# Kernel tuning notes

Measured on AMD Instinct MI355X. Metric: run time of the kernel, lower is better.

Reference implementation:

```python
import jax, jax.numpy as jnp
import numpy as np


def setup_inputs() -> dict:
    key = jax.random.key(0)
    B, C, H, W = 32, 256, 64, 64
    x = jax.random.normal(key, (B, C, H, W), dtype=jnp.float32)
    adj = jnp.ones((C, C), dtype=jnp.float32)
    para = jnp.ones((1, C, H, W), dtype=jnp.float32)
    return {"x": x, "adj": adj, "para": para}


def reference(x, adj, para):
    B, C, H, W = x.shape
    fea = x.reshape(B, C, H * W)                     # [B, C, HW]
    c_adj = jnp.mean(x, axis=(2, 3))                 # global avg pool -> [B, C]
    # pairwise sigmoid-difference similarity, batched over B
    d = c_adj[:, None, :] - c_adj[:, :, None]        # t1 - t2: [B, C(i=row from t2), C(j=col from t1)]
    s = jnp.abs(jnp.abs(jax.nn.sigmoid(d) - 0.5) - 0.5) * 2.0
    s = (s + jnp.swapaxes(s, 1, 2)) * 0.5            # symmetrize
    w = adj[None, :, :] * s                          # [B, C, C]
    out = jnp.einsum('bij,bjk->bik', w, fea)         # small GEMM per sample
    out = out.reshape(B, C, H, W) * para             # elementwise scale
    return jax.nn.relu(out)
```

## Files before the change

### kernel.cpp

```cpp
#include <hip/hip_runtime.h>
#include <math.h>

#define BB 32
#define CC 256
#define HWW 4096

typedef unsigned short u16;
typedef unsigned int u32;

typedef __attribute__((ext_vector_type(8))) short bf16x8;
typedef __attribute__((ext_vector_type(4))) float f32x4;

__device__ inline u16 f2bf(float f) {
    u32 u = __float_as_uint(f);
    u32 r = (u + 0x7fff + ((u >> 16) & 1)) >> 16;
    return (u16)r;
}


__global__ __launch_bounds__(256) void pool_transpose_kernel(const float* __restrict__ x,
                                                             u16* __restrict__ xT,
                                                             float* __restrict__ partial) {
    int b  = blockIdx.z;
    int c0 = blockIdx.y * 64;
    int h0 = blockIdx.x * 64;
    const float* xB = x + (size_t)b * CC * HWW;

    __shared__ float tile[64][65];
    __shared__ float psum[64];
    int t  = threadIdx.x;
    int cl = t >> 4;
    int h4 = (t & 15) * 4;

#pragma unroll
    for (int m = 0; m < 4; ++m) {
        int c = cl + 16 * m;
        float4 v = *(const float4*)&xB[(size_t)(c0 + c) * HWW + h0 + h4];
        tile[c][h4 + 0] = v.x;
        tile[c][h4 + 1] = v.y;
        tile[c][h4 + 2] = v.z;
        tile[c][h4 + 3] = v.w;
        float s = v.x + v.y + v.z + v.w;
#pragma unroll
        for (int off = 8; off > 0; off >>= 1)
            s += __shfl_down(s, off, 16);
        if ((t & 15) == 0) psum[c] = s;
    }
    __syncthreads();

    if (t < 64)
        partial[((size_t)b * 64 + blockIdx.x) * CC + c0 + t] = psum[t];

    int hl = t >> 2;
    int cq = (t & 3) * 16;
    u32 p0 = (u32)f2bf(tile[cq + 0][hl]) | ((u32)f2bf(tile[cq + 1][hl]) << 16);
    u32 p1 = (u32)f2bf(tile[cq + 2][hl]) | ((u32)f2bf(tile[cq + 3][hl]) << 16);
    u32 p2 = (u32)f2bf(tile[cq + 4][hl]) | ((u32)f2bf(tile[cq + 5][hl]) << 16);
    u32 p3 = (u32)f2bf(tile[cq + 6][hl]) | ((u32)f2bf(tile[cq + 7][hl]) << 16);
    u32 p4 = (u32)f2bf(tile[cq + 8][hl]) | ((u32)f2bf(tile[cq + 9][hl]) << 16);
    u32 p5 = (u32)f2bf(tile[cq +10][hl]) | ((u32)f2bf(tile[cq +11][hl]) << 16);
    u32 p6 = (u32)f2bf(tile[cq +12][hl]) | ((u32)f2bf(tile[cq +13][hl]) << 16);
    u32 p7 = (u32)f2bf(tile[cq +14][hl]) | ((u32)f2bf(tile[cq +15][hl]) << 16);
    u16* dst = xT + ((size_t)b * HWW + h0 + hl) * CC + c0 + cq;
    *(uint4*)(dst)     = make_uint4(p0, p1, p2, p3);
    *(uint4*)(dst + 8) = make_uint4(p4, p5, p6, p7);
}


__global__ __launch_bounds__(256) void reduce_kernel(const float* __restrict__ partial,
                                                     float* __restrict__ c_adj) {
    int b = blockIdx.x;
    int c = threadIdx.x;
    float s = 0.f;
#pragma unroll 8
    for (int hx = 0; hx < 64; ++hx)
        s += partial[((size_t)b * 64 + hx) * CC + c];
    c_adj[b * CC + c] = s * (1.0f / HWW);
}


__global__ __launch_bounds__(256) void weight_bf16_kernel(const float* __restrict__ c_adj,
                                                          const float* __restrict__ adj,
                                                          u16* __restrict__ wb) {
    int idx = blockIdx.x * 256 + threadIdx.x;
    int b = idx >> 16;
    int rem = idx & 65535;
    int i = rem >> 8;
    int j = rem & 255;
    float d = c_adj[b * CC + j] - c_adj[b * CC + i];
    float tt = expf(-fabsf(d));
    float s = 2.f * tt / (1.f + tt);
    wb[idx] = f2bf(adj[i * CC + j] * s);
}

#define GBM 128
#define GBN 128
#define GBK 32

__global__ __launch_bounds__(256) void mfma_gemm_kernel(const u16* __restrict__ wb,
                                                        const u16* __restrict__ xT,
                                                        const float* __restrict__ para,
                                                        float* __restrict__ out) {
    int b  = blockIdx.z;
    int i0 = blockIdx.y * GBM;
    int n0 = blockIdx.x * GBN;
    const u16* wB = wb + (size_t)b * CC * CC;
    const u16* xB = xT + (size_t)b * HWW * CC;

    __shared__ u16 lds[2][2][4096];

    int t    = threadIdx.x;
    int lane = t & 63;
    int wid  = t >> 6;
    int wr   = wid >> 1;
    int wc   = wid & 1;

    f32x4 acc[4][4] = {};

    int r0  = t >> 2;
    int c0q = t & 3;
    int cs  = c0q ^ ((r0 >> 1) & 3);
    int e0 = r0 * 32 + 8 * cs;
    int e1 = (r0 + 64) * 32 + 8 * cs;

    const u16* gA0 = wB + (size_t)(i0 + r0) * CC + 8 * c0q;
    const u16* gA1 = wB + (size_t)(i0 + r0 + 64) * CC + 8 * c0q;
    const u16* gB0 = xB + (size_t)(n0 + r0) * CC + 8 * c0q;
    const u16* gB1 = xB + (size_t)(n0 + r0 + 64) * CC + 8 * c0q;

    uint4 ra0, ra1, rb0, rb1;

#define LOADT(kk) { ra0 = *(const uint4*)(gA0 + (kk)); ra1 = *(const uint4*)(gA1 + (kk)); \
                    rb0 = *(const uint4*)(gB0 + (kk)); rb1 = *(const uint4*)(gB1 + (kk)); }
#define STORET(bf) { *(uint4*)&lds[bf][0][e0] = ra0; *(uint4*)&lds[bf][0][e1] = ra1; \
                     *(uint4*)&lds[bf][1][e0] = rb0; *(uint4*)&lds[bf][1][e1] = rb1; }

    LOADT(0);
    STORET(0);
    __syncthreads();

    int lrow = lane & 15;
    int kc   = lane >> 4;
    int swz  = (lrow >> 1) & 3;

#pragma unroll 1
    for (int kt = 0; kt < 8; ++kt) {
        int cur = kt & 1;
        if (kt < 7) LOADT((kt + 1) * GBK);

        bf16x8 af[4], bfr[4];
#pragma unroll
        for (int m = 0; m < 4; ++m) {
            int row = wr * 64 + m * 16 + lrow;
            af[m] = *(bf16x8*)&lds[cur][0][row * 32 + 8 * (kc ^ swz)];
        }
#pragma unroll
        for (int q = 0; q < 4; ++q) {
            int row = wc * 64 + q * 16 + lrow;
            bfr[q] = *(bf16x8*)&lds[cur][1][row * 32 + 8 * (kc ^ swz)];
        }
#pragma unroll
        for (int m = 0; m < 4; ++m)
#pragma unroll
            for (int q = 0; q < 4; ++q)
                acc[m][q] = __builtin_amdgcn_mfma_f32_16x16x32_bf16(af[m], bfr[q], acc[m][q], 0, 0, 0);

        if (kt < 7) STORET(cur ^ 1);
        __syncthreads();
    }
#undef LOADT
#undef STORET

    int dcol = lane & 15;
    int drow = 4 * (lane >> 4);
#pragma unroll
    for (int m = 0; m < 4; ++m) {
#pragma unroll
        for (int q = 0; q < 4; ++q) {
            int i = i0 + wr * 64 + m * 16 + drow;
            int n = n0 + wc * 64 + q * 16 + dcol;
#pragma unroll
            for (int r = 0; r < 4; ++r) {
                float pv = para[(size_t)(i + r) * HWW + n];
                float o = fmaxf(acc[m][q][r] * pv, 0.f);
                __builtin_nontemporal_store(o, &out[((size_t)b * CC + i + r) * HWW + n]);
            }
        }
    }
}


__global__ __launch_bounds__(256) void avgpool_kernel(const float* __restrict__ x,
                                                      float* __restrict__ c_adj) {
    int bc = blockIdx.x;
    const float4* p4 = (const float4*)(x + (size_t)bc * HWW);
    int t = threadIdx.x;
    float sum = 0.f;
#pragma unroll
    for (int m = 0; m < 4; ++m) {
        float4 v = p4[t + 256 * m];
        sum += v.x + v.y + v.z + v.w;
    }
#pragma unroll
    for (int off = 32; off > 0; off >>= 1)
        sum += __shfl_down(sum, off, 64);
    __shared__ float partial[4];
    int wid = t >> 6, lane = t & 63;
    if (lane == 0) partial[wid] = sum;
    __syncthreads();
    if (t == 0)
        c_adj[bc] = (partial[0] + partial[1] + partial[2] + partial[3]) * (1.0f / HWW);
}

__global__ __launch_bounds__(256) void weight_kernel(const float* __restrict__ c_adj,
                                                     const float* __restrict__ adj,
                                                     float* __restrict__ w) {
    int idx = blockIdx.x * 256 + threadIdx.x;
    int b = idx >> 16, rem = idx & 65535, i = rem >> 8, j = rem & 255;
    float d = c_adj[b * CC + j] - c_adj[b * CC + i];
    float tt = expf(-fabsf(d));
    w[idx] = adj[i * CC + j] * 2.f * tt / (1.f + tt);
}

#define BM 64
#define BN 64
#define BK 16
__global__ __launch_bounds__(256) void gemm_kernel(const float* __restrict__ w,
                                                   const float* __restrict__ x,
                                                   const float* __restrict__ para,
                                                   float* __restrict__ out) {
    int b = blockIdx.z, i0 = blockIdx.y * BM, n0 = blockIdx.x * BN;
    const float* wB = w + (size_t)b * CC * CC;
    const float* xB = x + (size_t)b * CC * HWW;
    float* outB = out + (size_t)b * CC * HWW;
    __shared__ float wT[BK][68];
    __shared__ float xS[BK][BN];
    int t = threadIdx.x, tr = t >> 4, tc = t & 15;
    float acc[4][4] = {};
    for (int k0 = 0; k0 < CC; k0 += BK) {
        {
            int i = t >> 2, kq = (t & 3) * 4;
            float4 v = *(const float4*)&wB[(size_t)(i0 + i) * CC + k0 + kq];
            wT[kq + 0][i] = v.x; wT[kq + 1][i] = v.y; wT[kq + 2][i] = v.z; wT[kq + 3][i] = v.w;
        }
        {
            int k = t >> 4, nq = (t & 15) * 4;
            *(float4*)&xS[k][nq] = *(const float4*)&xB[(size_t)(k0 + k) * HWW + n0 + nq];
        }
        __syncthreads();
#pragma unroll
        for (int k = 0; k < BK; ++k) {
            float wv[4], xv[4];
            *(float4*)wv = *(const float4*)&wT[k][tr * 4];
            *(float4*)xv = *(const float4*)&xS[k][tc * 4];
#pragma unroll
            for (int r = 0; r < 4; ++r)
#pragma unroll
                for (int q = 0; q < 4; ++q)
                    acc[r][q] = fmaf(wv[r], xv[q], acc[r][q]);
        }
        __syncthreads();
    }
#pragma unroll
    for (int r = 0; r < 4; ++r) {
        int i = i0 + tr * 4 + r, n = n0 + tc * 4;
        float4 pv = *(const float4*)&para[(size_t)i * HWW + n];
        float4 o;
        o.x = fmaxf(acc[r][0] * pv.x, 0.f);
        o.y = fmaxf(acc[r][1] * pv.y, 0.f);
        o.z = fmaxf(acc[r][2] * pv.z, 0.f);
        o.w = fmaxf(acc[r][3] * pv.w, 0.f);
        *(float4*)&outB[(size_t)i * HWW + n] = o;
    }
}


extern "C" void kernel_launch(void* const* d_in, const int* in_sizes, int n_in,
                              void* d_out, int out_size, void* d_ws, size_t ws_size,
                              hipStream_t stream) {
    const float* x    = (const float*)d_in[0];
    const float* adj  = (const float*)d_in[1];
    const float* para = (const float*)d_in[2];
    float* out = (float*)d_out;

    const size_t XT_BYTES = (size_t)BB * HWW * CC * 2;
    const size_t WB_BYTES = (size_t)BB * CC * CC * 2;
    const size_t CA_BYTES = (size_t)BB * CC * 4;
    const size_t REQ = XT_BYTES + WB_BYTES + CA_BYTES;

    if (ws_size >= REQ) {
        u16*   xT      = (u16*)d_ws;
        u16*   wbuf    = (u16*)((char*)d_ws + XT_BYTES);
        float* partial = (float*)((char*)d_ws + XT_BYTES);
        float* c_adj   = (float*)((char*)d_ws + XT_BYTES + WB_BYTES);

        dim3 gA(HWW / 64, CC / 64, BB);
        pool_transpose_kernel<<<gA, 256, 0, stream>>>(x, xT, partial);
        reduce_kernel<<<BB, 256, 0, stream>>>(partial, c_adj);
        weight_bf16_kernel<<<(BB * CC * CC) / 256, 256, 0, stream>>>(c_adj, adj, wbuf);
        dim3 gC(HWW / GBN, CC / GBM, BB);
        mfma_gemm_kernel<<<gC, 256, 0, stream>>>(wbuf, xT, para, out);
    } else {
        float* c_adj = (float*)d_ws;
        float* w     = (float*)d_ws + (BB * CC);
        avgpool_kernel<<<BB * CC, 256, 0, stream>>>(x, c_adj);
        weight_kernel<<<(BB * CC * CC) / 256, 256, 0, stream>>>(c_adj, adj, w);
        dim3 grid(HWW / BN, CC / BM, BB);
        gemm_kernel<<<grid, 256, 0, stream>>>(w, x, para, out);
    }
}
```

Baseline: 96.76 us.

## Fuse reduce and weight kernels; stage GEMM tiles via direct global-to-LDS loads

Merges the channel-mean reduction and the bf16 weight computation into one kernel, so each block recomputes its batch's channel means in shared memory and writes 32 rows of weights. This removes a launch and the round trip of c_adj through global memory. The partial buffer moves to its own workspace region because it previously aliased the weight buffer. The MFMA GEMM now uses global_load_lds to copy tiles straight into LDS, dropping the register staging and explicit LDS stores, with the swizzle moved into the global addresses.

Measured after the change: 93.28 us. -3.6%, faster.

```diff
diff --git a/kernel.cpp b/kernel.cpp
--- a/kernel.cpp
+++ b/kernel.cpp
@@ -67,30 +67,31 @@
 }
 
 
-__global__ __launch_bounds__(256) void reduce_kernel(const float* __restrict__ partial,
-                                                     float* __restrict__ c_adj) {
-    int b = blockIdx.x;
-    int c = threadIdx.x;
+__global__ __launch_bounds__(256) void reduce_weight_kernel(const float* __restrict__ partial,
+                                                            const float* __restrict__ adj,
+                                                            u16* __restrict__ wb) {
+    int b  = blockIdx.x >> 3;
+    int ic = (blockIdx.x & 7) * 32;
+    int t  = threadIdx.x;
+
+    __shared__ float ca[CC];
     float s = 0.f;
 #pragma unroll 8
     for (int hx = 0; hx < 64; ++hx)
-        s += partial[((size_t)b * 64 + hx) * CC + c];
-    c_adj[b * CC + c] = s * (1.0f / HWW);
-}
-
-
-__global__ __launch_bounds__(256) void weight_bf16_kernel(const float* __restrict__ c_adj,
-                                                          const float* __restrict__ adj,
-                                                          u16* __restrict__ wb) {
-    int idx = blockIdx.x * 256 + threadIdx.x;
-    int b = idx >> 16;
-    int rem = idx & 65535;
-    int i = rem >> 8;
-    int j = rem & 255;
-    float d = c_adj[b * CC + j] - c_adj[b * CC + i];
-    float tt = expf(-fabsf(d));
-    float s = 2.f * tt / (1.f + tt);
-    wb[idx] = f2bf(adj[i * CC + j] * s);
+        s += partial[((size_t)b * 64 + hx) * CC + t];
+    ca[t] = s * (1.0f / HWW);
+    __syncthreads();
+
+    u16* wB = wb + (size_t)b * CC * CC;
+    float cj = ca[t];
+#pragma unroll 4
+    for (int r = 0; r < 32; ++r) {
+        int i = ic + r;
+        float d  = cj - ca[i];
+        float tt = __expf(-fabsf(d));
+        float sv = 2.f * tt / (1.f + tt);
+        wB[(size_t)i * CC + t] = f2bf(adj[i * CC + t] * sv);
+    }
 }
 
 #define GBM 128
@@ -112,6 +113,7 @@
     int t    = threadIdx.x;
     int lane = t & 63;
     int wid  = t >> 6;
+    int wid_s = __builtin_amdgcn_readfirstlane(wid);
     int wr   = wid >> 1;
     int wc   = wid & 1;
 
@@ -119,24 +121,24 @@
 
     int r0  = t >> 2;
     int c0q = t & 3;
-    int cs  = c0q ^ ((r0 >> 1) & 3);
-    int e0 = r0 * 32 + 8 * cs;
-    int e1 = (r0 + 64) * 32 + 8 * cs;
-
-    const u16* gA0 = wB + (size_t)(i0 + r0) * CC + 8 * c0q;
-    const u16* gA1 = wB + (size_t)(i0 + r0 + 64) * CC + 8 * c0q;
-    const u16* gB0 = xB + (size_t)(n0 + r0) * CC + 8 * c0q;
-    const u16* gB1 = xB + (size_t)(n0 + r0 + 64) * CC + 8 * c0q;
-
-    uint4 ra0, ra1, rb0, rb1;
-
-#define LOADT(kk) { ra0 = *(const uint4*)(gA0 + (kk)); ra1 = *(const uint4*)(gA1 + (kk)); \
-                    rb0 = *(const uint4*)(gB0 + (kk)); rb1 = *(const uint4*)(gB1 + (kk)); }
-#define STORET(bf) { *(uint4*)&lds[bf][0][e0] = ra0; *(uint4*)&lds[bf][0][e1] = ra1; \
-                     *(uint4*)&lds[bf][1][e0] = rb0; *(uint4*)&lds[bf][1][e1] = rb1; }
-
-    LOADT(0);
-    STORET(0);
+    int csq = c0q ^ ((r0 >> 1) & 3);
+
+    const u16* gA0 = wB + (size_t)(i0 + r0) * CC + 8 * csq;
+    const u16* gA1 = wB + (size_t)(i0 + r0 + 64) * CC + 8 * csq;
+    const u16* gB0 = xB + (size_t)(n0 + r0) * CC + 8 * csq;
+    const u16* gB1 = xB + (size_t)(n0 + r0 + 64) * CC + 8 * csq;
+
+#define GLDS(ptr, dst) __builtin_amdgcn_global_load_lds( \
+        (const __attribute__((address_space(1))) void*)(ptr), \
+        (__attribute__((address_space(3))) void*)(dst), 16, 0, 0)
+
+#define STAGE(kk, bf) { \
+        GLDS(gA0 + (kk), &lds[bf][0][wid_s * 512]); \
+        GLDS(gA1 + (kk), &lds[bf][0][2048 + wid_s * 512]); \
+        GLDS(gB0 + (kk), &lds[bf][1][wid_s * 512]); \
+        GLDS(gB1 + (kk), &lds[bf][1][2048 + wid_s * 512]); }
+
+    STAGE(0, 0);
     __syncthreads();
 
     int lrow = lane & 15;
@@ -146,7 +148,7 @@
 #pragma unroll 1
     for (int kt = 0; kt < 8; ++kt) {
         int cur = kt & 1;
-        if (kt < 7) LOADT((kt + 1) * GBK);
+        if (kt < 7) STAGE((kt + 1) * GBK, cur ^ 1);
 
         bf16x8 af[4], bfr[4];
 #pragma unroll
@@ -165,11 +167,10 @@
             for (int q = 0; q < 4; ++q)
                 acc[m][q] = __builtin_amdgcn_mfma_f32_16x16x32_bf16(af[m], bfr[q], acc[m][q], 0, 0, 0);
 
-        if (kt < 7) STORET(cur ^ 1);
         __syncthreads();
     }
-#undef LOADT
-#undef STORET
+#undef STAGE
+#undef GLDS
 
     int dcol = lane & 15;
     int drow = 4 * (lane >> 4);
@@ -285,19 +286,17 @@
 
     const size_t XT_BYTES = (size_t)BB * HWW * CC * 2;
     const size_t WB_BYTES = (size_t)BB * CC * CC * 2;
-    const size_t CA_BYTES = (size_t)BB * CC * 4;
-    const size_t REQ = XT_BYTES + WB_BYTES + CA_BYTES;
+    const size_t PT_BYTES = (size_t)BB * 64 * CC * 4;
+    const size_t REQ = XT_BYTES + WB_BYTES + PT_BYTES;
 
     if (ws_size >= REQ) {
         u16*   xT      = (u16*)d_ws;
         u16*   wbuf    = (u16*)((char*)d_ws + XT_BYTES);
-        float* partial = (float*)((char*)d_ws + XT_BYTES);
-        float* c_adj   = (float*)((char*)d_ws + XT_BYTES + WB_BYTES);
+        float* partial = (float*)((char*)d_ws + XT_BYTES + WB_BYTES);
 
         dim3 gA(HWW / 64, CC / 64, BB);
         pool_transpose_kernel<<<gA, 256, 0, stream>>>(x, xT, partial);
-        reduce_kernel<<<BB, 256, 0, stream>>>(partial, c_adj);
-        weight_bf16_kernel<<<(BB * CC * CC) / 256, 256, 0, stream>>>(c_adj, adj, wbuf);
+        reduce_weight_kernel<<<BB * 8, 256, 0, stream>>>(partial, adj, wbuf);
         dim3 gC(HWW / GBN, CC / GBM, BB);
         mfma_gemm_kernel<<<gC, 256, 0, stream>>>(wbuf, xT, para, out);
     } else {
```
